# Kernel tuning notes

Measured on AMD Instinct MI355X. Metric: run time of the kernel, lower is better.

The kernel has to match this reference:

```python
import jax, jax.numpy as jnp
import numpy as np

B, T, C, H = 8, 2048, 1024, 64


def build_rope_cache(seq_len, dim):
    half = dim // 2
    inv_freq = 1.0 / (10000.0 ** (jnp.arange(half, dtype=jnp.float32) / half))
    t = jnp.arange(seq_len, dtype=jnp.float32)
    freqs = t[:, None] * inv_freq[None, :]          # (T, half)
    cos = jnp.repeat(jnp.cos(freqs), 2, axis=-1)    # (T, dim) interleaved
    sin = jnp.repeat(jnp.sin(freqs), 2, axis=-1)
    return cos, sin


def apply_rope(x, cos, sin):
    # x: (B, T, H); cos/sin: (T, H)
    x1 = x[..., ::2]
    x2 = x[..., 1::2]
    rot = jnp.stack([-x2, x1], axis=-1).reshape(x.shape)
    return x * cos[None] + rot * sin[None]


def setup_inputs() -> dict:
    key = jax.random.key(0)
    kx, kq, kk, kv = jax.random.split(key, 4)
    scale = 1.0 / np.sqrt(C)
    return {
        "x": jax.random.normal(kx, (B, T, C), dtype=jnp.float32),
        "Wq": jax.random.normal(kq, (C, H), dtype=jnp.float32) * scale,
        "Wk": jax.random.normal(kk, (C, H), dtype=jnp.float32) * scale,
        "Wv": jax.random.normal(kv, (C, H), dtype=jnp.float32) * scale,
    }


def reference(x, Wq, Wk, Wv):
    Bc, Tc, _ = x.shape
    head_size = Wq.shape[1]
    cos, sin = build_rope_cache(Tc, head_size)

    q = apply_rope(x @ Wq, cos, sin)   # (B, T, H)
    k = apply_rope(x @ Wk, cos, sin)   # (B, T, H)
    v = x @ Wv                          # (B, T, H)

    # full TxT masked softmax attention (matches original non-fused path)
    wei = jnp.einsum('bth,bsh->bts', q, k) * (head_size ** -0.5)  # (B, T, T)
    causal = jnp.tril(jnp.ones((Tc, Tc), dtype=bool))
    wei = jnp.where(causal[None], wei, -jnp.inf)
    wei = jax.nn.softmax(wei, axis=-1)
    # dropout p=0 (eval mode) -> identity
    return jnp.einsum('bts,bsh->bth', wei, v)
```

## Files before the change

kernel.cpp:

```cpp
#include <hip/hip_runtime.h>
#include <cmath>

#define Tn  2048
#define Cn  1024
#define Hn  64
#define BTn 16384

typedef _Float16 f16x8 __attribute__((ext_vector_type(8)));
typedef _Float16 f16x4 __attribute__((ext_vector_type(4)));
typedef _Float16 f16x2 __attribute__((ext_vector_type(2)));
typedef float    f32x4 __attribute__((ext_vector_type(4)));

__global__ __launch_bounds__(256) void prep_w_kernel(
    const float* __restrict__ Wq, const float* __restrict__ Wk,
    const float* __restrict__ Wv, _Float16* __restrict__ Wt)
{
    __shared__ float ts[64][65];
    const int blk = blockIdx.x;
    const int p   = blk >> 4;
    const int c0  = (blk & 15) * 64;
    const float* __restrict__ W = (p == 0) ? Wq : (p == 1) ? Wk : Wv;
    const int tid = threadIdx.x;
    #pragma unroll
    for (int it = 0; it < 16; it++) {
        int idx = tid + it * 256;
        int c = idx >> 6, n = idx & 63;
        ts[c][n] = W[(size_t)(c0 + c) * Hn + n];
    }
    __syncthreads();
    #pragma unroll
    for (int it = 0; it < 16; it++) {
        int idx = tid + it * 256;
        int n = idx >> 6, c = idx & 63;
        Wt[(size_t)(p * 64 + n) * Cn + c0 + c] = (_Float16)ts[c][n];
    }
}

#define XS2 520

__global__ __launch_bounds__(256, 4) void proj_kernel(
    const float* __restrict__ x, const _Float16* __restrict__ Wt,
    _Float16* __restrict__ qh, _Float16* __restrict__ kh, _Float16* __restrict__ vT)
{
    __shared__ _Float16 xs[32 * XS2];
    const int row0 = blockIdx.x * 32;
    const int tid  = threadIdx.x;
    const int wave = tid >> 6, lane = tid & 63;
    const int quad = lane >> 4, l15 = lane & 15;

    f32x4 acc[2][3] = {};
    const _Float16* __restrict__ wb = Wt + (size_t)(wave * 48 + l15) * Cn + quad * 8;

    #pragma unroll
    for (int ph = 0; ph < 2; ph++) {
        if (ph) __syncthreads();
        #pragma unroll 8
        for (int it = 0; it < 16; it++) {
            int idx = tid + it * 256;
            int r = idx >> 7, c4 = idx & 127;
            float4 xv = *(const float4*)&x[(size_t)(row0 + r) * Cn + ph * 512 + c4 * 4];
            f16x4 hv = { (_Float16)xv.x, (_Float16)xv.y, (_Float16)xv.z, (_Float16)xv.w };
            *(f16x4*)&xs[r * XS2 + c4 * 4] = hv;
        }
        __syncthreads();

        const _Float16* __restrict__ wp = wb + ph * 512;
        #pragma unroll 4
        for (int kc = 0; kc < 512; kc += 32) {
            f16x8 b0 = *(const f16x8*)&wp[kc];
            f16x8 b1 = *(const f16x8*)&wp[16 * Cn + kc];
            f16x8 b2 = *(const f16x8*)&wp[32 * Cn + kc];
            f16x8 a0 = *(const f16x8*)&xs[(     l15) * XS2 + kc + quad * 8];
            f16x8 a1 = *(const f16x8*)&xs[(16 + l15) * XS2 + kc + quad * 8];
            acc[0][0] = __builtin_amdgcn_mfma_f32_16x16x32_f16(a0, b0, acc[0][0], 0, 0, 0);
            acc[1][0] = __builtin_amdgcn_mfma_f32_16x16x32_f16(a1, b0, acc[1][0], 0, 0, 0);
            acc[0][1] = __builtin_amdgcn_mfma_f32_16x16x32_f16(a0, b1, acc[0][1], 0, 0, 0);
            acc[1][1] = __builtin_amdgcn_mfma_f32_16x16x32_f16(a1, b1, acc[1][1], 0, 0, 0);
            acc[0][2] = __builtin_amdgcn_mfma_f32_16x16x32_f16(a0, b2, acc[0][2], 0, 0, 0);
            acc[1][2] = __builtin_amdgcn_mfma_f32_16x16x32_f16(a1, b2, acc[1][2], 0, 0, 0);
        }
    }

    const int bidx = row0 >> 11;
    #pragma unroll
    for (int nt = 0; nt < 3; nt++) {
        const int n = wave * 48 + nt * 16 + l15;
        const int p = n >> 6;
        const int h = n & 63;
        if (p < 2) {
            _Float16* __restrict__ outb = (p == 0) ? qh : kh;
            const float invf = __expf(-0.2878231366242557f * (float)(h >> 1));
            #pragma unroll
            for (int mt = 0; mt < 2; mt++) {
                #pragma unroll
                for (int r = 0; r < 4; r++) {
                    int   row = row0 + mt * 16 + quad * 4 + r;
                    float val = acc[mt][nt][r];
                    float partner = __shfl_xor(val, 1, 64);
                    float ang = (float)(row & (Tn - 1)) * invf;
                    float sv, cv;
                    __sincosf(ang, &sv, &cv);
                    float res = (h & 1) ? fmaf(val, cv,  partner * sv)
                                        : fmaf(val, cv, -partner * sv);
                    if (p == 0) res *= 0.125f;
                    float resn = __shfl_xor(res, 1, 64);
                    if (!(l15 & 1)) {
                        f16x2 pk = { (_Float16)res, (_Float16)resn };
                        *(f16x2*)&outb[(size_t)row * Hn + h] = pk;
                    }
                }
            }
        } else {
            #pragma unroll
            for (int mt = 0; mt < 2; mt++) {
                int t = (row0 & (Tn - 1)) + mt * 16 + quad * 4;
                f16x4 pv = { (_Float16)acc[mt][nt][0], (_Float16)acc[mt][nt][1],
                             (_Float16)acc[mt][nt][2], (_Float16)acc[mt][nt][3] };
                *(f16x4*)&vT[((size_t)bidx * Hn + h) * Tn + t] = pv;
            }
        }
    }
}

#define PSP 72

__global__ __launch_bounds__(256, 4) void attn_kernel(
    const _Float16* __restrict__ qh, const _Float16* __restrict__ kh,
    const _Float16* __restrict__ vT, float* __restrict__ out)
{
    __shared__ _Float16 ps[4][16 * PSP];
    __shared__ float ocomb[4][16][65];
    __shared__ float mlcomb[4][2][16];

    const int blk = blockIdx.x;
    const int b   = blk & 7;
    const int j   = blk >> 3;
    const int jm  = j & 31, g = j >> 5;
    const int qt  = (g == 0) ? (127 - jm)
                  : (g == 1) ? (64 + jm)
                  : (g == 2) ? (63 - jm) : jm;
    const int t0  = qt * 16;
    const int tid = threadIdx.x;
    const int w = tid >> 6, lane = tid & 63;
    const int quad = lane >> 4, l15 = lane & 15;

    const _Float16* __restrict__ qb = qh + (size_t)b * Tn * Hn;
    const _Float16* __restrict__ kb = kh + (size_t)b * Tn * Hn;
    const _Float16* __restrict__ vb = vT + (size_t)b * Hn * Tn;

    const f16x8 aq0 = *(const f16x8*)&qb[(size_t)(t0 + l15) * Hn +      quad * 8];
    const f16x8 aq1 = *(const f16x8*)&qb[(size_t)(t0 + l15) * Hn + 32 + quad * 8];

    float m_run[4], l_run[4];
    f32x4 oacc[4] = {};
    #pragma unroll
    for (int r = 0; r < 4; r++) { m_run[r] = -1e30f; l_run[r] = 0.0f; }

    const int nst = (t0 + 16 + 63) >> 6;
    for (int jt = w; jt < nst; jt += 4) {
        const int s0 = jt * 64;

        f16x8 kf[4][2];
        #pragma unroll
        for (int nt = 0; nt < 4; nt++) {
            const _Float16* kp = &kb[(size_t)(s0 + nt * 16 + l15) * Hn + quad * 8];
            kf[nt][0] = *(const f16x8*)kp;
            kf[nt][1] = *(const f16x8*)(kp + 32);
        }
        f32x4 sacc[4];
        #pragma unroll
        for (int nt = 0; nt < 4; nt++) {
            f32x4 z = {};
            z = __builtin_amdgcn_mfma_f32_16x16x32_f16(aq0, kf[nt][0], z, 0, 0, 0);
            z = __builtin_amdgcn_mfma_f32_16x16x32_f16(aq1, kf[nt][1], z, 0, 0, 0);
            sacc[nt] = z;
        }

        f16x8 vf[2][4];
        #pragma unroll
        for (int sc = 0; sc < 2; sc++)
            #pragma unroll
            for (int ht = 0; ht < 4; ht++)
                vf[sc][ht] = *(const f16x8*)&vb[(size_t)(ht * 16 + l15) * Tn
                                                + s0 + sc * 32 + quad * 8];

        if (jt == nst - 1) {
            #pragma unroll
            for (int nt = 0; nt < 4; nt++)
                #pragma unroll
                for (int r = 0; r < 4; r++) {
                    int scol = s0 + nt * 16 + l15;
                    int trow = t0 + quad * 4 + r;
                    if (scol > trow) sacc[nt][r] = -1e30f;
                }
        }

        float pr[4][4];
        #pragma unroll
        for (int r = 0; r < 4; r++) {
            float mx = fmaxf(fmaxf(sacc[0][r], sacc[1][r]),
                             fmaxf(sacc[2][r], sacc[3][r]));
            #pragma unroll
            for (int off = 1; off < 16; off <<= 1)
                mx = fmaxf(mx, __shfl_xor(mx, off, 64));
            float mnew  = fmaxf(m_run[r], mx);
            float alpha = __expf(m_run[r] - mnew);
            m_run[r] = mnew;
            float rs = 0.0f;
            #pragma unroll
            for (int nt = 0; nt < 4; nt++) {
                float pv = __expf(sacc[nt][r] - mnew);
                pr[nt][r] = pv; rs += pv;
            }
            #pragma unroll
            for (int off = 1; off < 16; off <<= 1)
                rs += __shfl_xor(rs, off, 64);
            l_run[r] = fmaf(l_run[r], alpha, rs);
            #pragma unroll
            for (int ht = 0; ht < 4; ht++)
                oacc[ht][r] = oacc[ht][r] * alpha;
        }

        #pragma unroll
        for (int nt = 0; nt < 4; nt++)
            #pragma unroll
            for (int r = 0; r < 4; r++) {
                float pv = pr[nt][r];
                float pn = __shfl_xor(pv, 1, 64);
                if (!(l15 & 1)) {
                    f16x2 pk = { (_Float16)pv, (_Float16)pn };
                    *(f16x2*)&ps[w][(quad * 4 + r) * PSP + nt * 16 + l15] = pk;
                }
            }

        #pragma unroll
        for (int sc = 0; sc < 2; sc++) {
            f16x8 ap = *(const f16x8*)&ps[w][l15 * PSP + sc * 32 + quad * 8];
            #pragma unroll
            for (int ht = 0; ht < 4; ht++)
                oacc[ht] = __builtin_amdgcn_mfma_f32_16x16x32_f16(ap, vf[sc][ht],
                                                                  oacc[ht], 0, 0, 0);
        }
    }

    #pragma unroll
    for (int r = 0; r < 4; r++) {
        #pragma unroll
        for (int ht = 0; ht < 4; ht++)
            ocomb[w][quad * 4 + r][ht * 16 + l15] = oacc[ht][r];
        if (l15 == 0) {
            mlcomb[w][0][quad * 4 + r] = m_run[r];
            mlcomb[w][1][quad * 4 + r] = l_run[r];
        }
    }
    __syncthreads();

    #pragma unroll
    for (int rp = 0; rp < 4; rp++) {
        int row = w * 4 + rp;
        float m0 = mlcomb[0][0][row], m1 = mlcomb[1][0][row];
        float m2 = mlcomb[2][0][row], m3 = mlcomb[3][0][row];
        float mm = fmaxf(fmaxf(m0, m1), fmaxf(m2, m3));
        float a0 = __expf(m0 - mm), a1 = __expf(m1 - mm);
        float a2 = __expf(m2 - mm), a3 = __expf(m3 - mm);
        float ll = mlcomb[0][1][row] * a0 + mlcomb[1][1][row] * a1
                 + mlcomb[2][1][row] * a2 + mlcomb[3][1][row] * a3;
        float ov = (ocomb[0][row][lane] * a0 + ocomb[1][row][lane] * a1
                  + ocomb[2][row][lane] * a2 + ocomb[3][row][lane] * a3) / ll;
        out[((size_t)b * Tn + t0 + row) * Hn + lane] = ov;
    }
}

extern "C" void kernel_launch(void* const* d_in, const int* in_sizes, int n_in,
                              void* d_out, int out_size, void* d_ws, size_t ws_size,
                              hipStream_t stream) {
    const float* x  = (const float*)d_in[0];
    const float* Wq = (const float*)d_in[1];
    const float* Wk = (const float*)d_in[2];
    const float* Wv = (const float*)d_in[3];

    const size_t qkvN = (size_t)BTn * Hn;
    _Float16* qh = (_Float16*)d_ws;
    _Float16* kh = qh + qkvN;
    _Float16* vT = kh + qkvN;
    _Float16* Wt = vT + qkvN;

    prep_w_kernel<<<48, 256, 0, stream>>>(Wq, Wk, Wv, Wt);
    proj_kernel<<<BTn / 32, 256, 0, stream>>>(x, Wt, qh, kh, vT);
    attn_kernel<<<1024, 256, 0, stream>>>(qh, kh, vT, (float*)d_out);
}
```

Baseline: 157.8 us.

## Split projection K dimension across two wave groups with shared-memory reduction

The projection kernel moves to 512 threads per block. The whole 32x1024 x tile is loaded into LDS in one pass instead of two half passes, and the two 4-wave groups each handle half of the K dimension. Partial accumulators from the upper group are reduced through LDS before the RoPE epilogue. This doubles wave-level parallelism and removes a mid-loop sync, at the cost of about 66KB of LDS per block, which may limit occupancy, plus an extra reduction step.

```diff
diff --git a/kernel.cpp b/kernel.cpp
--- a/kernel.cpp
+++ b/kernel.cpp
@@ -36,59 +36,75 @@
     }
 }
 
-#define XS2 520
-
-__global__ __launch_bounds__(256, 4) void proj_kernel(
+#define XSP 1032
+
+__global__ __launch_bounds__(512, 4) void proj_kernel(
     const float* __restrict__ x, const _Float16* __restrict__ Wt,
-    _Float16* __restrict__ qh, _Float16* __restrict__ kh, _Float16* __restrict__ vT)
+    _Float16* __restrict__ qh, _Float16* __restrict__ kh_out, _Float16* __restrict__ vT)
 {
-    __shared__ _Float16 xs[32 * XS2];
+    __shared__ __align__(16) _Float16 xs[32 * XSP];
     const int row0 = blockIdx.x * 32;
     const int tid  = threadIdx.x;
     const int wave = tid >> 6, lane = tid & 63;
+    const int kh   = wave >> 2;
+    const int wc   = wave & 3;
     const int quad = lane >> 4, l15 = lane & 15;
 
+    #pragma unroll 8
+    for (int it = 0; it < 16; it++) {
+        int idx = tid + it * 512;
+        int r = idx >> 8, c4 = idx & 255;
+        float4 xv = *(const float4*)&x[(size_t)(row0 + r) * Cn + c4 * 4];
+        f16x4 hv = { (_Float16)xv.x, (_Float16)xv.y, (_Float16)xv.z, (_Float16)xv.w };
+        *(f16x4*)&xs[r * XSP + c4 * 4] = hv;
+    }
+    __syncthreads();
+
     f32x4 acc[2][3] = {};
-    const _Float16* __restrict__ wb = Wt + (size_t)(wave * 48 + l15) * Cn + quad * 8;
-
-    #pragma unroll
-    for (int ph = 0; ph < 2; ph++) {
-        if (ph) __syncthreads();
-        #pragma unroll 8
-        for (int it = 0; it < 16; it++) {
-            int idx = tid + it * 256;
-            int r = idx >> 7, c4 = idx & 127;
-            float4 xv = *(const float4*)&x[(size_t)(row0 + r) * Cn + ph * 512 + c4 * 4];
-            f16x4 hv = { (_Float16)xv.x, (_Float16)xv.y, (_Float16)xv.z, (_Float16)xv.w };
-            *(f16x4*)&xs[r * XS2 + c4 * 4] = hv;
-        }
-        __syncthreads();
-
-        const _Float16* __restrict__ wp = wb + ph * 512;
-        #pragma unroll 4
-        for (int kc = 0; kc < 512; kc += 32) {
-            f16x8 b0 = *(const f16x8*)&wp[kc];
-            f16x8 b1 = *(const f16x8*)&wp[16 * Cn + kc];
-            f16x8 b2 = *(const f16x8*)&wp[32 * Cn + kc];
-            f16x8 a0 = *(const f16x8*)&xs[(     l15) * XS2 + kc + quad * 8];
-            f16x8 a1 = *(const f16x8*)&xs[(16 + l15) * XS2 + kc + quad * 8];
-            acc[0][0] = __builtin_amdgcn_mfma_f32_16x16x32_f16(a0, b0, acc[0][0], 0, 0, 0);
-            acc[1][0] = __builtin_amdgcn_mfma_f32_16x16x32_f16(a1, b0, acc[1][0], 0, 0, 0);
-            acc[0][1] = __builtin_amdgcn_mfma_f32_16x16x32_f16(a0, b1, acc[0][1], 0, 0, 0);
-            acc[1][1] = __builtin_amdgcn_mfma_f32_16x16x32_f16(a1, b1, acc[1][1], 0, 0, 0);
-            acc[0][2] = __builtin_amdgcn_mfma_f32_16x16x32_f16(a0, b2, acc[0][2], 0, 0, 0);
-            acc[1][2] = __builtin_amdgcn_mfma_f32_16x16x32_f16(a1, b2, acc[1][2], 0, 0, 0);
-        }
-    }
+    const _Float16* __restrict__ wb = Wt + (size_t)(wc * 48 + l15) * Cn
+                                         + kh * 512 + quad * 8;
+    const _Float16* __restrict__ xp = &xs[kh * 512 + quad * 8];
+
+    #pragma unroll 4
+    for (int kc = 0; kc < 512; kc += 32) {
+        f16x8 b0 = *(const f16x8*)&wb[kc];
+        f16x8 b1 = *(const f16x8*)&wb[16 * Cn + kc];
+        f16x8 b2 = *(const f16x8*)&wb[32 * Cn + kc];
+        f16x8 a0 = *(const f16x8*)&xp[(     l15) * XSP + kc];
+        f16x8 a1 = *(const f16x8*)&xp[(16 + l15) * XSP + kc];
+        acc[0][0] = __builtin_amdgcn_mfma_f32_16x16x32_f16(a0, b0, acc[0][0], 0, 0, 0);
+        acc[1][0] = __builtin_amdgcn_mfma_f32_16x16x32_f16(a1, b0, acc[1][0], 0, 0, 0);
+        acc[0][1] = __builtin_amdgcn_mfma_f32_16x16x32_f16(a0, b1, acc[0][1], 0, 0, 0);
+        acc[1][1] = __builtin_amdgcn_mfma_f32_16x16x32_f16(a1, b1, acc[1][1], 0, 0, 0);
+        acc[0][2] = __builtin_amdgcn_mfma_f32_16x16x32_f16(a0, b2, acc[0][2], 0, 0, 0);
+        acc[1][2] = __builtin_amdgcn_mfma_f32_16x16x32_f16(a1, b2, acc[1][2], 0, 0, 0);
+    }
+
+    __syncthreads();
+    f32x4* __restrict__ pbuf = (f32x4*)xs;
+    if (kh) {
+        #pragma unroll
+        for (int mt = 0; mt < 2; mt++)
+            #pragma unroll
+            for (int nt = 0; nt < 3; nt++)
+                pbuf[(mt * 3 + nt) * 256 + wc * 64 + lane] = acc[mt][nt];
+    }
+    __syncthreads();
+    if (kh) return;
+    #pragma unroll
+    for (int mt = 0; mt < 2; mt++)
+        #pragma unroll
+        for (int nt = 0; nt < 3; nt++)
+            acc[mt][nt] += pbuf[(mt * 3 + nt) * 256 + wc * 64 + lane];
 
     const int bidx = row0 >> 11;
     #pragma unroll
     for (int nt = 0; nt < 3; nt++) {
-        const int n = wave * 48 + nt * 16 + l15;
+        const int n = wc * 48 + nt * 16 + l15;
         const int p = n >> 6;
         const int h = n & 63;
         if (p < 2) {
-            _Float16* __restrict__ outb = (p == 0) ? qh : kh;
+            _Float16* __restrict__ outb = (p == 0) ? qh : kh_out;
             const float invf = __expf(-0.2878231366242557f * (float)(h >> 1));
             #pragma unroll
             for (int mt = 0; mt < 2; mt++) {
@@ -286,6 +302,6 @@
     _Float16* Wt = vT + qkvN;
 
     prep_w_kernel<<<48, 256, 0, stream>>>(Wq, Wk, Wv, Wt);
-    proj_kernel<<<BTn / 32, 256, 0, stream>>>(x, Wt, qh, kh, vT);
+    proj_kernel<<<BTn / 32, 512, 0, stream>>>(x, Wt, qh, kh, vT);
     attn_kernel<<<1024, 256, 0, stream>>>(qh, kh, vT, (float*)d_out);
 }
```

Result: no change. 155.6 us (-1.4%).
